# Optimization experiments

Measured on AMD Instinct MI355X. Metric: run time of the kernel, lower is better.

Reference implementation:

```python
import jax, jax.numpy as jnp
import numpy as np

B, N, DIN, DOUT = 8, 2048, 128, 128

def setup_inputs() -> dict:
    key = jax.random.key(0)
    k1, k2, k3, k4 = jax.random.split(key, 4)
    x = jax.random.normal(k1, (B, N, DIN), dtype=jnp.float32)
    adj = jax.random.uniform(k2, (B, N, N), dtype=jnp.float32)
    W = jax.random.normal(k3, (DIN, DOUT), dtype=jnp.float32) / np.sqrt(DIN)
    b = jax.random.normal(k4, (DOUT,), dtype=jnp.float32) * 0.01
    return {"x": x, "adj": adj, "W": W, "b": b}

def reference(x, adj, W, b):
    # degree over last dim of adj: [B, N]
    degree = jnp.sum(adj, axis=2)
    d_norm = 1.0 / jnp.sqrt(degree + 1e-8)
    # D^{-1/2} A D^{-1/2} == row/col elementwise scaling (same math as diag_embed+bmm)
    adj_norm = d_norm[:, :, None] * adj * d_norm[:, None, :]
    support = jnp.einsum('bnm,bmd->bnd', adj_norm, x)  # [B, N, DIN]
    return support @ W + b  # [B, N, DOUT]
```

## Files before the change

kernel.cpp:

```cpp
#include <hip/hip_runtime.h>
#include <hip/hip_bf16.h>

#define NN 2048
#define DD 128

typedef __attribute__((ext_vector_type(4))) float f32x4;
typedef __attribute__((ext_vector_type(8))) short short8;
typedef __attribute__((ext_vector_type(2))) unsigned int u32x2;

__device__ __forceinline__ unsigned short f2bf_bits(float f) {
  union { __hip_bfloat16 h; unsigned short s; } u;
  u.h = __float2bfloat16(f);
  return u.s;
}

__device__ __forceinline__ short8 cvt8(f32x4 a, f32x4 b) {
  short8 r;
  r[0] = (short)f2bf_bits(a[0]); r[1] = (short)f2bf_bits(a[1]);
  r[2] = (short)f2bf_bits(a[2]); r[3] = (short)f2bf_bits(a[3]);
  r[4] = (short)f2bf_bits(b[0]); r[5] = (short)f2bf_bits(b[1]);
  r[6] = (short)f2bf_bits(b[2]); r[7] = (short)f2bf_bits(b[3]);
  return r;
}

__device__ __forceinline__ u32x2 pack4(f32x4 v) {
  u32x2 u;
  u[0] = (unsigned)f2bf_bits(v[0]) | ((unsigned)f2bf_bits(v[1]) << 16);
  u[1] = (unsigned)f2bf_bits(v[2]) | ((unsigned)f2bf_bits(v[3]) << 16);
  return u;
}

__global__ void k_degree(const float* __restrict__ adj, float* __restrict__ dnorm) {
  const int wv = threadIdx.x >> 6;
  const int ln = threadIdx.x & 63;
  const int row = blockIdx.x * 4 + wv;
  const f32x4* rowp = (const f32x4*)(adj + (size_t)row * NN);
  float s = 0.0f;
#pragma unroll
  for (int i = 0; i < 8; ++i) {
    f32x4 v = rowp[i * 64 + ln];
    s += v[0] + v[1] + v[2] + v[3];
  }
#pragma unroll
  for (int off = 32; off >= 1; off >>= 1) s += __shfl_xor(s, off);
  if (ln == 0) dnorm[row] = rsqrtf(s + 1e-8f);
}

__global__ void k_y(const float* __restrict__ x, const float* __restrict__ W,
                    const float* __restrict__ dnorm, short* __restrict__ yT) {
  const int ln = threadIdx.x & 63;
  const int wv = threadIdx.x >> 6;
  const int bb = blockIdx.x >> 5;
  const int n0 = (blockIdx.x & 31) << 6;
  const int l15 = ln & 15, l4 = ln >> 4;
  const int dbase = wv * 32;

  short8 af[2][4];
#pragma unroll
  for (int dt = 0; dt < 2; ++dt)
#pragma unroll
    for (int ks = 0; ks < 4; ++ks) {
      short8 a;
#pragma unroll
      for (int j = 0; j < 8; ++j)
        a[j] = (short)f2bf_bits(W[(size_t)(ks * 32 + l4 * 8 + j) * DD + dbase + dt * 16 + l15]);
      af[dt][ks] = a;
    }

  f32x4 acc[2][4];
#pragma unroll
  for (int dt = 0; dt < 2; ++dt)
#pragma unroll
    for (int nt = 0; nt < 4; ++nt) acc[dt][nt] = (f32x4)0.0f;

  const float* xb = x + (size_t)bb * NN * DD;
  const float* dnb = dnorm + (size_t)bb * NN;
#pragma unroll
  for (int nt = 0; nt < 4; ++nt) {
    const int n = n0 + nt * 16 + l15;
    const float dn = dnb[n];
#pragma unroll
    for (int ks = 0; ks < 4; ++ks) {
      f32x4 p = *(const f32x4*)(xb + (size_t)n * DD + ks * 32 + l4 * 8);
      f32x4 q = *(const f32x4*)(xb + (size_t)n * DD + ks * 32 + l4 * 8 + 4);
      short8 bf = cvt8(p * dn, q * dn);
#pragma unroll
      for (int dt = 0; dt < 2; ++dt)
        acc[dt][nt] = __builtin_amdgcn_mfma_f32_16x16x32_bf16(af[dt][ks], bf, acc[dt][nt], 0, 0, 0);
    }
  }

  short* yb = yT + (size_t)bb * DD * NN;
#pragma unroll
  for (int dt = 0; dt < 2; ++dt)
#pragma unroll
    for (int nt = 0; nt < 4; ++nt)
#pragma unroll
      for (int rr = 0; rr < 4; ++rr) {
        int d = dbase + dt * 16 + l4 * 4 + rr;
        yb[(size_t)d * NN + n0 + nt * 16 + l15] = (short)f2bf_bits(acc[dt][nt][rr]);
      }
}

__launch_bounds__(512, 4)
__global__ void k_gemm(const float* __restrict__ adj, const short* __restrict__ yT,
                       const float* __restrict__ dnorm, const float* __restrict__ bias,
                       float* __restrict__ out) {
  __shared__ short As[4][2048];

  const int t = threadIdx.x;
  const int ln = t & 63;
  const int wv = t >> 6;
  const int orig = ((blockIdx.x & 7) << 6) | (blockIdx.x >> 3);
  const int bb = orig >> 6;
  const int m0 = (orig & 63) << 5;

  const float* ablk = adj + ((size_t)bb * NN + m0) * NN;
  const int oc = (wv << 4) + (ln & 15);
  const int kg8 = (ln >> 4) << 3;
  const short* ybase = yT + ((size_t)bb * DD + oc) * NN;

  const unsigned srow = (unsigned)t >> 4;
  const unsigned sc4 = ((unsigned)t & 15u) << 2;

  f32x4 acc[2];
  acc[0] = (f32x4)0.0f; acc[1] = (f32x4)0.0f;

  auto loadA = [&](int tile) -> f32x4 {
    return *(const f32x4*)(ablk + (size_t)srow * NN + (tile << 6) + sc4);
  };
  auto loadB = [&](int tile, int ks) -> short8 {
    return *(const short8*)(ybase + (tile << 6) + ks * 32 + kg8);
  };
  auto writeA = [&](f32x4 v, int buf) {
    unsigned byte = (srow << 7) + (sc4 << 1);
    byte ^= (srow & 7u) << 4;
    *(u32x2*)((char*)As + (buf << 12) + byte) = pack4(v);
  };
  auto compute = [&](int buf, short8 b0, short8 b1) {
    const char* base = (const char*)As + (buf << 12);
#pragma unroll
    for (int ks = 0; ks < 2; ++ks) {
      short8 bf = ks ? b1 : b0;
#pragma unroll
      for (int m = 0; m < 2; ++m) {
        unsigned row = (unsigned)(m * 16 + (ln & 15));
        unsigned byte = (row << 7) + (unsigned)((ks * 32 + kg8) << 1);
        byte ^= (row & 7u) << 4;
        short8 a = *(const short8*)(base + byte);
        acc[m] = __builtin_amdgcn_mfma_f32_16x16x32_bf16(a, bf, acc[m], 0, 0, 0);
      }
    }
  };

  f32x4 sA0 = loadA(0), sA1 = loadA(1), sA2 = loadA(2), sA3 = loadA(3);
  f32x4 sA4 = loadA(4), sA5 = loadA(5), sA6 = loadA(6), sA7 = loadA(7);
  short8 b0k0 = loadB(0, 0), b0k1 = loadB(0, 1);
  short8 b1k0 = loadB(1, 0), b1k1 = loadB(1, 1);
  short8 b2k0 = loadB(2, 0), b2k1 = loadB(2, 1);
  short8 b3k0 = loadB(3, 0), b3k1 = loadB(3, 1);
  writeA(sA0, 0);
  asm volatile("s_waitcnt lgkmcnt(0)\n\ts_barrier" ::: "memory");

#define GITER(T, SNEW, SWR, BK0, BK1)                                 \
  {                                                                   \
    if ((T) < 24) SNEW = loadA((T) + 8);                              \
    short8 nb0 = BK0, nb1 = BK1;                                      \
    if ((T) < 28) { nb0 = loadB((T) + 4, 0); nb1 = loadB((T) + 4, 1); } \
    writeA(SWR, ((T) + 1) & 3);                                       \
    asm volatile("s_waitcnt lgkmcnt(0)\n\ts_barrier" ::: "memory");   \
    compute((T) & 3, BK0, BK1);                                       \
    BK0 = nb0; BK1 = nb1;                                             \
  }

#pragma unroll 1
  for (int t8 = 0; t8 < 32; t8 += 8) {
    GITER(t8 + 0, sA0, sA1, b0k0, b0k1);
    GITER(t8 + 1, sA1, sA2, b1k0, b1k1);
    GITER(t8 + 2, sA2, sA3, b2k0, b2k1);
    GITER(t8 + 3, sA3, sA4, b3k0, b3k1);
    GITER(t8 + 4, sA4, sA5, b0k0, b0k1);
    GITER(t8 + 5, sA5, sA6, b1k0, b1k1);
    GITER(t8 + 6, sA6, sA7, b2k0, b2k1);
    GITER(t8 + 7, sA7, sA0, b3k0, b3k1);
  }
#undef GITER

  const float bv = bias[oc];
  const int rbase = (ln >> 4) << 2;
#pragma unroll
  for (int m = 0; m < 2; ++m) {
    f32x4 dn = *(const f32x4*)(dnorm + (size_t)bb * NN + m0 + m * 16 + rbase);
#pragma unroll
    for (int rr = 0; rr < 4; ++rr)
      out[(size_t)(bb * NN + m0 + m * 16 + rbase + rr) * DD + oc] = acc[m][rr] * dn[rr] + bv;
  }
}

extern "C" void kernel_launch(void* const* d_in, const int* in_sizes, int n_in,
                              void* d_out, int out_size, void* d_ws, size_t ws_size,
                              hipStream_t stream) {
  (void)in_sizes; (void)n_in; (void)out_size; (void)ws_size;
  const float* x = (const float*)d_in[0];
  const float* adj = (const float*)d_in[1];
  const float* W = (const float*)d_in[2];
  const float* bias = (const float*)d_in[3];
  float* out = (float*)d_out;

  char* ws = (char*)d_ws;
  float* dnorm = (float*)ws;
  short* yT = (short*)(ws + (1 << 16));

  k_degree<<<4096, 256, 0, stream>>>(adj, dnorm);
  k_y<<<256, 256, 0, stream>>>(x, W, dnorm, yT);
  k_gemm<<<512, 512, 0, stream>>>(adj, yT, dnorm, bias, out);
}
```

Before: 67.88 us.

## Fuse degree, projection and aggregation into one cooperative kernel with grid sync

Merges the three kernels (degree reduction, dnorm-scaled x@W projection, adjacency GEMM) into a single cooperative launch. Each block computes the degree of its own 32 rows into shared memory, produces the matching slice of yT, then waits on a grid-wide sync before running the unchanged pipelined GEMM. The aim is to remove two kernel launch gaps and keep dnorm local to the block. The cost is a grid barrier and an extra read of the block's adj rows before the GEMM. If the cooperative launch fails, the code falls back to the old three kernels.

New measurement: 132.6 us. +95.3%, slower.

```diff
diff --git a/kernel.cpp b/kernel.cpp
--- a/kernel.cpp
+++ b/kernel.cpp
@@ -1,8 +1,11 @@
 #include <hip/hip_runtime.h>
 #include <hip/hip_bf16.h>
+#include <hip/hip_cooperative_groups.h>
 
 #define NN 2048
 #define DD 128
+
+namespace cg = cooperative_groups;
 
 typedef __attribute__((ext_vector_type(4))) float f32x4;
 typedef __attribute__((ext_vector_type(8))) short short8;
@@ -30,96 +33,84 @@
   return u;
 }
 
-__global__ void k_degree(const float* __restrict__ adj, float* __restrict__ dnorm) {
-  const int wv = threadIdx.x >> 6;
-  const int ln = threadIdx.x & 63;
-  const int row = blockIdx.x * 4 + wv;
-  const f32x4* rowp = (const f32x4*)(adj + (size_t)row * NN);
-  float s = 0.0f;
-#pragma unroll
-  for (int i = 0; i < 8; ++i) {
-    f32x4 v = rowp[i * 64 + ln];
-    s += v[0] + v[1] + v[2] + v[3];
-  }
-#pragma unroll
-  for (int off = 32; off >= 1; off >>= 1) s += __shfl_xor(s, off);
-  if (ln == 0) dnorm[row] = rsqrtf(s + 1e-8f);
-}
-
-__global__ void k_y(const float* __restrict__ x, const float* __restrict__ W,
-                    const float* __restrict__ dnorm, short* __restrict__ yT) {
-  const int ln = threadIdx.x & 63;
-  const int wv = threadIdx.x >> 6;
-  const int bb = blockIdx.x >> 5;
-  const int n0 = (blockIdx.x & 31) << 6;
-  const int l15 = ln & 15, l4 = ln >> 4;
-  const int dbase = wv * 32;
-
-  short8 af[2][4];
-#pragma unroll
-  for (int dt = 0; dt < 2; ++dt)
-#pragma unroll
-    for (int ks = 0; ks < 4; ++ks) {
-      short8 a;
-#pragma unroll
-      for (int j = 0; j < 8; ++j)
-        a[j] = (short)f2bf_bits(W[(size_t)(ks * 32 + l4 * 8 + j) * DD + dbase + dt * 16 + l15]);
-      af[dt][ks] = a;
-    }
-
-  f32x4 acc[2][4];
-#pragma unroll
-  for (int dt = 0; dt < 2; ++dt)
-#pragma unroll
-    for (int nt = 0; nt < 4; ++nt) acc[dt][nt] = (f32x4)0.0f;
-
-  const float* xb = x + (size_t)bb * NN * DD;
-  const float* dnb = dnorm + (size_t)bb * NN;
-#pragma unroll
-  for (int nt = 0; nt < 4; ++nt) {
-    const int n = n0 + nt * 16 + l15;
-    const float dn = dnb[n];
-#pragma unroll
-    for (int ks = 0; ks < 4; ++ks) {
-      f32x4 p = *(const f32x4*)(xb + (size_t)n * DD + ks * 32 + l4 * 8);
-      f32x4 q = *(const f32x4*)(xb + (size_t)n * DD + ks * 32 + l4 * 8 + 4);
-      short8 bf = cvt8(p * dn, q * dn);
-#pragma unroll
-      for (int dt = 0; dt < 2; ++dt)
-        acc[dt][nt] = __builtin_amdgcn_mfma_f32_16x16x32_bf16(af[dt][ks], bf, acc[dt][nt], 0, 0, 0);
-    }
-  }
-
-  short* yb = yT + (size_t)bb * DD * NN;
-#pragma unroll
-  for (int dt = 0; dt < 2; ++dt)
-#pragma unroll
-    for (int nt = 0; nt < 4; ++nt)
-#pragma unroll
-      for (int rr = 0; rr < 4; ++rr) {
-        int d = dbase + dt * 16 + l4 * 4 + rr;
-        yb[(size_t)d * NN + n0 + nt * 16 + l15] = (short)f2bf_bits(acc[dt][nt][rr]);
-      }
-}
-
 __launch_bounds__(512, 4)
-__global__ void k_gemm(const float* __restrict__ adj, const short* __restrict__ yT,
-                       const float* __restrict__ dnorm, const float* __restrict__ bias,
-                       float* __restrict__ out) {
+__global__ void k_all(const float* __restrict__ adj, const float* __restrict__ x,
+                      const float* __restrict__ W, const float* __restrict__ bias,
+                      float* __restrict__ out, short* __restrict__ yT) {
   __shared__ short As[4][2048];
+  __shared__ float dnl[32];
 
   const int t = threadIdx.x;
   const int ln = t & 63;
   const int wv = t >> 6;
+  const int l15 = ln & 15, l4 = ln >> 4;
+
   const int orig = ((blockIdx.x & 7) << 6) | (blockIdx.x >> 3);
   const int bb = orig >> 6;
   const int m0 = (orig & 63) << 5;
-
-  const float* ablk = adj + ((size_t)bb * NN + m0) * NN;
-  const int oc = (wv << 4) + (ln & 15);
-  const int kg8 = (ln >> 4) << 3;
+  const size_t rowg0 = (size_t)bb * NN + m0;
+
+  {
+    const int r = (wv << 2) + l4;
+    const float* arow = adj + (rowg0 + r) * NN + (l15 << 2);
+    float s = 0.f;
+#pragma unroll
+    for (int rd = 0; rd < 4; ++rd) {
+      f32x4 v[8];
+#pragma unroll
+      for (int j = 0; j < 8; ++j)
+        v[j] = *(const f32x4*)(arow + (rd * 8 + j) * 64);
+#pragma unroll
+      for (int j = 0; j < 8; ++j)
+        s += (v[j][0] + v[j][1]) + (v[j][2] + v[j][3]);
+    }
+    s += __shfl_xor(s, 1); s += __shfl_xor(s, 2);
+    s += __shfl_xor(s, 4); s += __shfl_xor(s, 8);
+    if (l15 == 0) dnl[r] = rsqrtf(s + 1e-8f);
+  }
+  __syncthreads();
+
+  {
+    const int dbase = (wv & 3) << 5;
+    const int nh = (wv >> 2) << 4;
+    const int nloc = nh + l15;
+    const float dn = dnl[nloc];
+    const float* xr = x + (rowg0 + nloc) * DD;
+    short8 af[2][4];
+#pragma unroll
+    for (int dt = 0; dt < 2; ++dt)
+#pragma unroll
+      for (int ks = 0; ks < 4; ++ks) {
+        short8 a;
+#pragma unroll
+        for (int j = 0; j < 8; ++j)
+          a[j] = (short)f2bf_bits(W[(size_t)(ks * 32 + l4 * 8 + j) * DD + dbase + dt * 16 + l15]);
+        af[dt][ks] = a;
+      }
+    f32x4 acc2[2]; acc2[0] = (f32x4)0.f; acc2[1] = (f32x4)0.f;
+#pragma unroll
+    for (int ks = 0; ks < 4; ++ks) {
+      f32x4 p = *(const f32x4*)(xr + ks * 32 + l4 * 8);
+      f32x4 q = *(const f32x4*)(xr + ks * 32 + l4 * 8 + 4);
+      short8 bf = cvt8(p * dn, q * dn);
+      acc2[0] = __builtin_amdgcn_mfma_f32_16x16x32_bf16(af[0][ks], bf, acc2[0], 0, 0, 0);
+      acc2[1] = __builtin_amdgcn_mfma_f32_16x16x32_bf16(af[1][ks], bf, acc2[1], 0, 0, 0);
+    }
+    short* yb = yT + (size_t)bb * DD * NN;
+#pragma unroll
+    for (int dt = 0; dt < 2; ++dt)
+#pragma unroll
+      for (int rr = 0; rr < 4; ++rr)
+        yb[(size_t)(dbase + dt * 16 + l4 * 4 + rr) * NN + m0 + nloc] =
+            (short)f2bf_bits(acc2[dt][rr]);
+  }
+
+  cg::this_grid().sync();
+
+  const float* ablk = adj + rowg0 * NN;
+  const int oc = (wv << 4) + l15;
+  const int kg8 = l4 << 3;
   const short* ybase = yT + ((size_t)bb * DD + oc) * NN;
-
   const unsigned srow = (unsigned)t >> 4;
   const unsigned sc4 = ((unsigned)t & 15u) << 2;
 
@@ -144,7 +135,7 @@
       short8 bf = ks ? b1 : b0;
 #pragma unroll
       for (int m = 0; m < 2; ++m) {
-        unsigned row = (unsigned)(m * 16 + (ln & 15));
+        unsigned row = (unsigned)(m * 16 + l15);
         unsigned byte = (row << 7) + (unsigned)((ks * 32 + kg8) << 1);
         byte ^= (row & 7u) << 4;
         short8 a = *(const short8*)(base + byte);
@@ -162,15 +153,15 @@
   writeA(sA0, 0);
   asm volatile("s_waitcnt lgkmcnt(0)\n\ts_barrier" ::: "memory");
 
-#define GITER(T, SNEW, SWR, BK0, BK1)                                 \
-  {                                                                   \
-    if ((T) < 24) SNEW = loadA((T) + 8);                              \
-    short8 nb0 = BK0, nb1 = BK1;                                      \
+#define GITER(T, SNEW, SWR, BK0, BK1)                                   \
+  {                                                                     \
+    if ((T) < 24) SNEW = loadA((T) + 8);                                \
+    short8 nb0 = BK0, nb1 = BK1;                                        \
     if ((T) < 28) { nb0 = loadB((T) + 4, 0); nb1 = loadB((T) + 4, 1); } \
-    writeA(SWR, ((T) + 1) & 3);                                       \
-    asm volatile("s_waitcnt lgkmcnt(0)\n\ts_barrier" ::: "memory");   \
-    compute((T) & 3, BK0, BK1);                                       \
-    BK0 = nb0; BK1 = nb1;                                             \
+    writeA(SWR, ((T) + 1) & 3);                                         \
+    asm volatile("s_waitcnt lgkmcnt(0)\n\ts_barrier" ::: "memory");     \
+    compute((T) & 3, BK0, BK1);                                         \
+    BK0 = nb0; BK1 = nb1;                                               \
   }
 
 #pragma unroll 1
@@ -187,6 +178,173 @@
 #undef GITER
 
   const float bv = bias[oc];
+  const int rb = l4 << 2;
+#pragma unroll
+  for (int m = 0; m < 2; ++m)
+#pragma unroll
+    for (int rr = 0; rr < 4; ++rr) {
+      const int row = m * 16 + rb + rr;
+      out[(rowg0 + row) * DD + oc] = acc[m][rr] * dnl[row] + bv;
+    }
+}
+
+__global__ void k_degree(const float* __restrict__ adj, float* __restrict__ dnorm) {
+  const int wv = threadIdx.x >> 6;
+  const int ln = threadIdx.x & 63;
+  const int row = blockIdx.x * 4 + wv;
+  const f32x4* rowp = (const f32x4*)(adj + (size_t)row * NN);
+  float s = 0.0f;
+#pragma unroll
+  for (int i = 0; i < 8; ++i) {
+    f32x4 v = rowp[i * 64 + ln];
+    s += v[0] + v[1] + v[2] + v[3];
+  }
+#pragma unroll
+  for (int off = 32; off >= 1; off >>= 1) s += __shfl_xor(s, off);
+  if (ln == 0) dnorm[row] = rsqrtf(s + 1e-8f);
+}
+
+__global__ void k_y(const float* __restrict__ x, const float* __restrict__ W,
+                    const float* __restrict__ dnorm, short* __restrict__ yT) {
+  const int ln = threadIdx.x & 63;
+  const int wv = threadIdx.x >> 6;
+  const int bb = blockIdx.x >> 5;
+  const int n0 = (blockIdx.x & 31) << 6;
+  const int l15 = ln & 15, l4 = ln >> 4;
+  const int dbase = wv * 32;
+
+  short8 af[2][4];
+#pragma unroll
+  for (int dt = 0; dt < 2; ++dt)
+#pragma unroll
+    for (int ks = 0; ks < 4; ++ks) {
+      short8 a;
+#pragma unroll
+      for (int j = 0; j < 8; ++j)
+        a[j] = (short)f2bf_bits(W[(size_t)(ks * 32 + l4 * 8 + j) * DD + dbase + dt * 16 + l15]);
+      af[dt][ks] = a;
+    }
+
+  f32x4 acc[2][4];
+#pragma unroll
+  for (int dt = 0; dt < 2; ++dt)
+#pragma unroll
+    for (int nt = 0; nt < 4; ++nt) acc[dt][nt] = (f32x4)0.0f;
+
+  const float* xb = x + (size_t)bb * NN * DD;
+  const float* dnb = dnorm + (size_t)bb * NN;
+#pragma unroll
+  for (int nt = 0; nt < 4; ++nt) {
+    const int n = n0 + nt * 16 + l15;
+    const float dn = dnb[n];
+#pragma unroll
+    for (int ks = 0; ks < 4; ++ks) {
+      f32x4 p = *(const f32x4*)(xb + (size_t)n * DD + ks * 32 + l4 * 8);
+      f32x4 q = *(const f32x4*)(xb + (size_t)n * DD + ks * 32 + l4 * 8 + 4);
+      short8 bf = cvt8(p * dn, q * dn);
+#pragma unroll
+      for (int dt = 0; dt < 2; ++dt)
+        acc[dt][nt] = __builtin_amdgcn_mfma_f32_16x16x32_bf16(af[dt][ks], bf, acc[dt][nt], 0, 0, 0);
+    }
+  }
+
+  short* yb = yT + (size_t)bb * DD * NN;
+#pragma unroll
+  for (int dt = 0; dt < 2; ++dt)
+#pragma unroll
+    for (int nt = 0; nt < 4; ++nt)
+#pragma unroll
+      for (int rr = 0; rr < 4; ++rr) {
+        int d = dbase + dt * 16 + l4 * 4 + rr;
+        yb[(size_t)d * NN + n0 + nt * 16 + l15] = (short)f2bf_bits(acc[dt][nt][rr]);
+      }
+}
+
+__launch_bounds__(512, 4)
+__global__ void k_gemm(const float* __restrict__ adj, const short* __restrict__ yT,
+                       const float* __restrict__ dnorm, const float* __restrict__ bias,
+                       float* __restrict__ out) {
+  __shared__ short As[4][2048];
+
+  const int t = threadIdx.x;
+  const int ln = t & 63;
+  const int wv = t >> 6;
+  const int orig = ((blockIdx.x & 7) << 6) | (blockIdx.x >> 3);
+  const int bb = orig >> 6;
+  const int m0 = (orig & 63) << 5;
+
+  const float* ablk = adj + ((size_t)bb * NN + m0) * NN;
+  const int oc = (wv << 4) + (ln & 15);
+  const int kg8 = (ln >> 4) << 3;
+  const short* ybase = yT + ((size_t)bb * DD + oc) * NN;
+
+  const unsigned srow = (unsigned)t >> 4;
+  const unsigned sc4 = ((unsigned)t & 15u) << 2;
+
+  f32x4 acc[2];
+  acc[0] = (f32x4)0.0f; acc[1] = (f32x4)0.0f;
+
+  auto loadA = [&](int tile) -> f32x4 {
+    return *(const f32x4*)(ablk + (size_t)srow * NN + (tile << 6) + sc4);
+  };
+  auto loadB = [&](int tile, int ks) -> short8 {
+    return *(const short8*)(ybase + (tile << 6) + ks * 32 + kg8);
+  };
+  auto writeA = [&](f32x4 v, int buf) {
+    unsigned byte = (srow << 7) + (sc4 << 1);
+    byte ^= (srow & 7u) << 4;
+    *(u32x2*)((char*)As + (buf << 12) + byte) = pack4(v);
+  };
+  auto compute = [&](int buf, short8 b0, short8 b1) {
+    const char* base = (const char*)As + (buf << 12);
+#pragma unroll
+    for (int ks = 0; ks < 2; ++ks) {
+      short8 bf = ks ? b1 : b0;
+#pragma unroll
+      for (int m = 0; m < 2; ++m) {
+        unsigned row = (unsigned)(m * 16 + (ln & 15));
+        unsigned byte = (row << 7) + (unsigned)((ks * 32 + kg8) << 1);
+        byte ^= (row & 7u) << 4;
+        short8 a = *(const short8*)(base + byte);
+        acc[m] = __builtin_amdgcn_mfma_f32_16x16x32_bf16(a, bf, acc[m], 0, 0, 0);
+      }
+    }
+  };
+
+  f32x4 sA0 = loadA(0), sA1 = loadA(1), sA2 = loadA(2), sA3 = loadA(3);
+  f32x4 sA4 = loadA(4), sA5 = loadA(5), sA6 = loadA(6), sA7 = loadA(7);
+  short8 b0k0 = loadB(0, 0), b0k1 = loadB(0, 1);
+  short8 b1k0 = loadB(1, 0), b1k1 = loadB(1, 1);
+  short8 b2k0 = loadB(2, 0), b2k1 = loadB(2, 1);
+  short8 b3k0 = loadB(3, 0), b3k1 = loadB(3, 1);
+  writeA(sA0, 0);
+  asm volatile("s_waitcnt lgkmcnt(0)\n\ts_barrier" ::: "memory");
+
+#define GITER(T, SNEW, SWR, BK0, BK1)                                   \
+  {                                                                     \
+    if ((T) < 24) SNEW = loadA((T) + 8);                                \
+    short8 nb0 = BK0, nb1 = BK1;                                        \
+    if ((T) < 28) { nb0 = loadB((T) + 4, 0); nb1 = loadB((T) + 4, 1); } \
+    writeA(SWR, ((T) + 1) & 3);                                         \
+    asm volatile("s_waitcnt lgkmcnt(0)\n\ts_barrier" ::: "memory");     \
+    compute((T) & 3, BK0, BK1);                                         \
+    BK0 = nb0; BK1 = nb1;                                               \
+  }
+
+#pragma unroll 1
+  for (int t8 = 0; t8 < 32; t8 += 8) {
+    GITER(t8 + 0, sA0, sA1, b0k0, b0k1);
+    GITER(t8 + 1, sA1, sA2, b1k0, b1k1);
+    GITER(t8 + 2, sA2, sA3, b2k0, b2k1);
+    GITER(t8 + 3, sA3, sA4, b3k0, b3k1);
+    GITER(t8 + 4, sA4, sA5, b0k0, b0k1);
+    GITER(t8 + 5, sA5, sA6, b1k0, b1k1);
+    GITER(t8 + 6, sA6, sA7, b2k0, b2k1);
+    GITER(t8 + 7, sA7, sA0, b3k0, b3k1);
+  }
+#undef GITER
+
+  const float bv = bias[oc];
   const int rbase = (ln >> 4) << 2;
 #pragma unroll
   for (int m = 0; m < 2; ++m) {
@@ -211,7 +369,14 @@
   float* dnorm = (float*)ws;
   short* yT = (short*)(ws + (1 << 16));
 
-  k_degree<<<4096, 256, 0, stream>>>(adj, dnorm);
-  k_y<<<256, 256, 0, stream>>>(x, W, dnorm, yT);
-  k_gemm<<<512, 512, 0, stream>>>(adj, yT, dnorm, bias, out);
-}
+  void* args[] = {(void*)&adj, (void*)&x, (void*)&W, (void*)&bias,
+                  (void*)&out, (void*)&yT};
+  hipError_t e = hipLaunchCooperativeKernel((const void*)k_all, dim3(512),
+                                            dim3(512), args, 0, stream);
+  if (e != hipSuccess) {
+    (void)hipGetLastError();
+    k_degree<<<4096, 256, 0, stream>>>(adj, dnorm);
+    k_y<<<256, 256, 0, stream>>>(x, W, dnorm, yT);
+    k_gemm<<<512, 512, 0, stream>>>(adj, yT, dnorm, bias, out);
+  }
+}
```

## Pre-scale and convert adjacency to bf16 in degree pass, GEMM reads bf16

Applied to the files above, without the earlier changes.

The degree kernel now keeps each adjacency row in registers, scales it by the row's D^-1/2 and writes a bf16 copy to workspace. The GEMM then streams that bf16 matrix instead of the fp32 adjacency and no longer converts or applies the row normalisation in its epilogue. The goal is to halve the GEMM's adjacency traffic, at the cost of an extra 64 MB bf16 write plus a re-read of that data, making total traffic roughly equal or higher. The copy's row scaling by the row's own norm matches the reference, which uses d_norm on rows.

Result: slower. 77.21 us (+13.8%).

```diff
diff --git a/kernel.cpp b/kernel.cpp
--- a/kernel.cpp
+++ b/kernel.cpp
@@ -23,27 +23,31 @@
   return r;
 }
 
-__device__ __forceinline__ u32x2 pack4(f32x4 v) {
-  u32x2 u;
-  u[0] = (unsigned)f2bf_bits(v[0]) | ((unsigned)f2bf_bits(v[1]) << 16);
-  u[1] = (unsigned)f2bf_bits(v[2]) | ((unsigned)f2bf_bits(v[3]) << 16);
-  return u;
-}
-
-__global__ void k_degree(const float* __restrict__ adj, float* __restrict__ dnorm) {
+__global__ void k_degcvt(const float* __restrict__ adj, float* __restrict__ dnorm,
+                         short* __restrict__ adjS) {
   const int wv = threadIdx.x >> 6;
   const int ln = threadIdx.x & 63;
   const int row = blockIdx.x * 4 + wv;
   const f32x4* rowp = (const f32x4*)(adj + (size_t)row * NN);
+  f32x4 v[8];
   float s = 0.0f;
 #pragma unroll
   for (int i = 0; i < 8; ++i) {
-    f32x4 v = rowp[i * 64 + ln];
-    s += v[0] + v[1] + v[2] + v[3];
+    v[i] = rowp[i * 64 + ln];
+    s += v[i][0] + v[i][1] + v[i][2] + v[i][3];
   }
 #pragma unroll
   for (int off = 32; off >= 1; off >>= 1) s += __shfl_xor(s, off);
-  if (ln == 0) dnorm[row] = rsqrtf(s + 1e-8f);
+  const float dn = rsqrtf(s + 1e-8f);
+  if (ln == 0) dnorm[row] = dn;
+  u32x2* orow = (u32x2*)(adjS + (size_t)row * NN);
+#pragma unroll
+  for (int i = 0; i < 8; ++i) {
+    u32x2 u;
+    u[0] = (unsigned)f2bf_bits(v[i][0] * dn) | ((unsigned)f2bf_bits(v[i][1] * dn) << 16);
+    u[1] = (unsigned)f2bf_bits(v[i][2] * dn) | ((unsigned)f2bf_bits(v[i][3] * dn) << 16);
+    orow[i * 64 + ln] = u;
+  }
 }
 
 __global__ void k_y(const float* __restrict__ x, const float* __restrict__ W,
@@ -103,9 +107,8 @@
 }
 
 __launch_bounds__(512, 4)
-__global__ void k_gemm(const float* __restrict__ adj, const short* __restrict__ yT,
-                       const float* __restrict__ dnorm, const float* __restrict__ bias,
-                       float* __restrict__ out) {
+__global__ void k_gemmS(const short* __restrict__ adjS, const short* __restrict__ yT,
+                        const float* __restrict__ bias, float* __restrict__ out) {
   __shared__ short As[4][2048];
 
   const int t = threadIdx.x;
@@ -115,27 +118,27 @@
   const int bb = orig >> 6;
   const int m0 = (orig & 63) << 5;
 
-  const float* ablk = adj + ((size_t)bb * NN + m0) * NN;
+  const short* ablk = adjS + ((size_t)bb * NN + m0) * NN;
   const int oc = (wv << 4) + (ln & 15);
   const int kg8 = (ln >> 4) << 3;
   const short* ybase = yT + ((size_t)bb * DD + oc) * NN;
 
   const unsigned srow = (unsigned)t >> 4;
-  const unsigned sc4 = ((unsigned)t & 15u) << 2;
+  const unsigned sc = ((unsigned)t & 15u) << 2;
 
   f32x4 acc[2];
   acc[0] = (f32x4)0.0f; acc[1] = (f32x4)0.0f;
 
-  auto loadA = [&](int tile) -> f32x4 {
-    return *(const f32x4*)(ablk + (size_t)srow * NN + (tile << 6) + sc4);
+  auto loadA = [&](int tile) -> u32x2 {
+    return *(const u32x2*)(ablk + (size_t)srow * NN + (tile << 6) + sc);
   };
   auto loadB = [&](int tile, int ks) -> short8 {
     return *(const short8*)(ybase + (tile << 6) + ks * 32 + kg8);
   };
-  auto writeA = [&](f32x4 v, int buf) {
-    unsigned byte = (srow << 7) + (sc4 << 1);
+  auto writeA = [&](u32x2 v, int buf) {
+    unsigned byte = (srow << 7) + (sc << 1);
     byte ^= (srow & 7u) << 4;
-    *(u32x2*)((char*)As + (buf << 12) + byte) = pack4(v);
+    *(u32x2*)((char*)As + (buf << 12) + byte) = v;
   };
   auto compute = [&](int buf, short8 b0, short8 b1) {
     const char* base = (const char*)As + (buf << 12);
@@ -153,8 +156,8 @@
     }
   };
 
-  f32x4 sA0 = loadA(0), sA1 = loadA(1), sA2 = loadA(2), sA3 = loadA(3);
-  f32x4 sA4 = loadA(4), sA5 = loadA(5), sA6 = loadA(6), sA7 = loadA(7);
+  u32x2 sA0 = loadA(0), sA1 = loadA(1), sA2 = loadA(2), sA3 = loadA(3);
+  u32x2 sA4 = loadA(4), sA5 = loadA(5), sA6 = loadA(6), sA7 = loadA(7);
   short8 b0k0 = loadB(0, 0), b0k1 = loadB(0, 1);
   short8 b1k0 = loadB(1, 0), b1k1 = loadB(1, 1);
   short8 b2k0 = loadB(2, 0), b2k1 = loadB(2, 1);
@@ -162,15 +165,15 @@
   writeA(sA0, 0);
   asm volatile("s_waitcnt lgkmcnt(0)\n\ts_barrier" ::: "memory");
 
-#define GITER(T, SNEW, SWR, BK0, BK1)                                 \
-  {                                                                   \
-    if ((T) < 24) SNEW = loadA((T) + 8);                              \
-    short8 nb0 = BK0, nb1 = BK1;                                      \
+#define GITER(T, SNEW, SWR, BK0, BK1)                                   \
+  {                                                                     \
+    if ((T) < 24) SNEW = loadA((T) + 8);                                \
+    short8 nb0 = BK0, nb1 = BK1;                                        \
     if ((T) < 28) { nb0 = loadB((T) + 4, 0); nb1 = loadB((T) + 4, 1); } \
-    writeA(SWR, ((T) + 1) & 3);                                       \
-    asm volatile("s_waitcnt lgkmcnt(0)\n\ts_barrier" ::: "memory");   \
-    compute((T) & 3, BK0, BK1);                                       \
-    BK0 = nb0; BK1 = nb1;                                             \
+    writeA(SWR, ((T) + 1) & 3);                                         \
+    asm volatile("s_waitcnt lgkmcnt(0)\n\ts_barrier" ::: "memory");     \
+    compute((T) & 3, BK0, BK1);                                         \
+    BK0 = nb0; BK1 = nb1;                                               \
   }
 
 #pragma unroll 1
@@ -189,12 +192,10 @@
   const float bv = bias[oc];
   const int rbase = (ln >> 4) << 2;
 #pragma unroll
-  for (int m = 0; m < 2; ++m) {
-    f32x4 dn = *(const f32x4*)(dnorm + (size_t)bb * NN + m0 + m * 16 + rbase);
+  for (int m = 0; m < 2; ++m)
 #pragma unroll
     for (int rr = 0; rr < 4; ++rr)
-      out[(size_t)(bb * NN + m0 + m * 16 + rbase + rr) * DD + oc] = acc[m][rr] * dn[rr] + bv;
-  }
+      out[(size_t)(bb * NN + m0 + m * 16 + rbase + rr) * DD + oc] = acc[m][rr] + bv;
 }
 
 extern "C" void kernel_launch(void* const* d_in, const int* in_sizes, int n_in,
@@ -210,8 +211,9 @@
   char* ws = (char*)d_ws;
   float* dnorm = (float*)ws;
   short* yT = (short*)(ws + (1 << 16));
-
-  k_degree<<<4096, 256, 0, stream>>>(adj, dnorm);
+  short* adjS = (short*)(ws + (1 << 16) + (4 << 20));
+
+  k_degcvt<<<4096, 256, 0, stream>>>(adj, dnorm, adjS);
   k_y<<<256, 256, 0, stream>>>(x, W, dnorm, yT);
-  k_gemm<<<512, 512, 0, stream>>>(adj, yT, dnorm, bias, out);
-}
+  k_gemmS<<<512, 512, 0, stream>>>(adjS, yT, bias, out);
+}
```
